# Optimization experiments

Measured on AMD Instinct MI355X. Metric: run time of the kernel, lower is better.

The kernel has to match this reference:

```python
import jax, jax.numpy as jnp
import numpy as np

D_MODEL = 256
D_INNER = 512
D_STATE = 16
DT_RANK = 16
D_CONV = 4
N_LAYERS = 2
L2_LAMBDA = 0.01


def _layernorm(x, g, b, eps=1e-5):
    mu = x.mean(-1, keepdims=True)
    var = x.var(-1, keepdims=True)
    return (x - mu) / jnp.sqrt(var + eps) * g + b


def _selective_scan(u, delta, A, Bm, C, D):
    # u, delta: (B, L, di); A: (di, ds); Bm, C: (B, L, ds); D: (di,)
    B_, L, di = u.shape
    ds = A.shape[1]

    def step(s, inp):
        d_t, u_t, b_t, c_t = inp  # (B,di),(B,di),(B,ds),(B,ds)
        dA = jnp.exp(d_t[..., None] * A)                      # (B,di,ds)
        s = s * dA + (d_t * u_t)[..., None] * b_t[:, None, :]  # (B,di,ds)
        y = jnp.einsum('bds,bs->bd', s, c_t)
        return s, y

    s0 = jnp.zeros((B_, di, ds), u.dtype)
    xs = (jnp.swapaxes(delta, 0, 1), jnp.swapaxes(u, 0, 1),
          jnp.swapaxes(Bm, 0, 1), jnp.swapaxes(C, 0, 1))
    _, ys = jax.lax.scan(step, s0, xs)  # ys: (L, B, di)
    return jnp.swapaxes(ys, 0, 1) + u * D


def _mamba_block(x, ng, nb, ipw, cw, cb, xpw, dtw, dtb, A_log, Dp, opw):
    h = _layernorm(x, ng, nb)
    xz = h @ ipw.T                       # (B,L,2*di)
    u, z = xz[..., :D_INNER], xz[..., D_INNER:]
    # causal depthwise conv along time
    uc = jnp.swapaxes(u, 1, 2)           # (B,di,L)
    uc = jax.lax.conv_general_dilated(
        uc, cw, window_strides=(1,), padding=[(D_CONV - 1, 0)],
        feature_group_count=D_INNER,
        dimension_numbers=('NCH', 'OIH', 'NCH')) + cb[None, :, None]
    u = jax.nn.silu(jnp.swapaxes(uc, 1, 2))
    xdbc = u @ xpw.T                     # (B,L,dt_rank+2*ds)
    dt = xdbc[..., :DT_RANK]
    Bm = xdbc[..., DT_RANK:DT_RANK + D_STATE]
    C = xdbc[..., DT_RANK + D_STATE:]
    delta = jax.nn.softplus(dt @ dtw.T + dtb)
    A = -jnp.exp(A_log)
    y = _selective_scan(u, delta, A, Bm, C, Dp)
    y = y * jax.nn.silu(z)
    return x + y @ opw.T


def setup_inputs() -> dict:
    key = jax.random.key(0)
    ks = jax.random.split(key, 24)
    s = 0.05
    inp = {
        'x': jax.random.normal(ks[0], (4, 1024, 768), jnp.float32),
        'in_w': jax.random.normal(ks[1], (D_MODEL, 768), jnp.float32) * s,
        'in_b': jnp.zeros((D_MODEL,), jnp.float32),
        'ln_g': jnp.ones((D_MODEL,), jnp.float32),
        'ln_b': jnp.zeros((D_MODEL,), jnp.float32),
        'blk_ng': jnp.ones((N_LAYERS, D_MODEL), jnp.float32),
        'blk_nb': jnp.zeros((N_LAYERS, D_MODEL), jnp.float32),
        'blk_ipw': jax.random.normal(ks[2], (N_LAYERS, 2 * D_INNER, D_MODEL), jnp.float32) * s,
        'blk_cw': jax.random.normal(ks[3], (N_LAYERS, D_INNER, 1, D_CONV), jnp.float32) * 0.2,
        'blk_cb': jnp.zeros((N_LAYERS, D_INNER), jnp.float32),
        'blk_xpw': jax.random.normal(ks[4], (N_LAYERS, DT_RANK + 2 * D_STATE, D_INNER), jnp.float32) * s,
        'blk_dtw': jax.random.normal(ks[5], (N_LAYERS, D_INNER, DT_RANK), jnp.float32) * s,
        'blk_dtb': jax.random.normal(ks[6], (N_LAYERS, D_INNER), jnp.float32) * 0.1,
        'blk_Alog': jax.random.uniform(ks[7], (N_LAYERS, D_INNER, D_STATE), jnp.float32, 0.0, 1.0),
        'blk_D': jnp.ones((N_LAYERS, D_INNER), jnp.float32),
        'blk_opw': jax.random.normal(ks[8], (N_LAYERS, D_MODEL, D_INNER), jnp.float32) * s,
        'op_w': jax.random.normal(ks[9], (D_MODEL, D_MODEL), jnp.float32) * s,
        'op_b': jnp.zeros((D_MODEL,), jnp.float32),
        'cls_w': jax.random.normal(ks[10], (128, D_MODEL), jnp.float32) * s,
        'cls_b': jnp.zeros((128,), jnp.float32),
    }
    return inp


def reference(x, in_w, in_b, ln_g, ln_b, blk_ng, blk_nb, blk_ipw, blk_cw, blk_cb,
              blk_xpw, blk_dtw, blk_dtb, blk_Alog, blk_D, blk_opw,
              op_w, op_b, cls_w, cls_b):
    h = x @ in_w.T + in_b
    h = _layernorm(h, ln_g, ln_b)
    h = jax.nn.gelu(h, approximate=False)
    # dropout is identity at inference
    for l in range(N_LAYERS):
        h = _mamba_block(h, blk_ng[l], blk_nb[l], blk_ipw[l], blk_cw[l], blk_cb[l],
                         blk_xpw[l], blk_dtw[l], blk_dtb[l], blk_Alog[l], blk_D[l], blk_opw[l])
    h = h @ op_w.T + op_b
    h = jax.nn.gelu(h, approximate=False)
    logits = h @ cls_w.T + cls_b
    l2_loss = L2_LAMBDA * jnp.mean(jnp.linalg.norm(h, axis=-1))
    return logits, l2_loss
```

## Files before the change

kernel.cpp:

```cpp
#include <hip/hip_runtime.h>
#include <hip/hip_bf16.h>
#include <math.h>

typedef __attribute__((ext_vector_type(8))) short frag8;
typedef __attribute__((ext_vector_type(4))) float f32x4;

__device__ __forceinline__ float gelu_exact(float x) {
    return 0.5f * x * (1.0f + erff(x * 0.70710678118654752f));
}
__device__ __forceinline__ float exp2_raw(float x) {
    return __builtin_amdgcn_exp2f(x);
}
__device__ __forceinline__ float softplus_f(float x) {
    float e = exp2_raw(x * 1.4426950408889634f);
    float sp = __log2f(1.0f + e) * 0.6931471805599453f;
    return (x > 20.0f) ? x : sp;
}
__device__ __forceinline__ float sigmoid_f(float x) {
    return 1.0f / (1.0f + __expf(-x));
}
__device__ __forceinline__ unsigned short bf16bits(float x) {
    __hip_bfloat16 h = __float2bfloat16(x);
    return *(unsigned short*)&h;
}
__device__ __forceinline__ float bf2f(unsigned short u) {
    unsigned int v = ((unsigned int)u) << 16;
    return __builtin_bit_cast(float, v);
}
__device__ __forceinline__ float row_sum16(float x) {
    int t;
    t = __builtin_amdgcn_update_dpp(0, __builtin_bit_cast(int, x), 0x128, 0xf, 0xf, true);
    x += __builtin_bit_cast(float, t);
    t = __builtin_amdgcn_update_dpp(0, __builtin_bit_cast(int, x), 0x124, 0xf, 0xf, true);
    x += __builtin_bit_cast(float, t);
    t = __builtin_amdgcn_update_dpp(0, __builtin_bit_cast(int, x), 0x122, 0xf, 0xf, true);
    x += __builtin_bit_cast(float, t);
    t = __builtin_amdgcn_update_dpp(0, __builtin_bit_cast(int, x), 0x121, 0xf, 0xf, true);
    x += __builtin_bit_cast(float, t);
    return x;
}
__device__ __forceinline__ float prefix_sum64(float x) {
    int t;
    t = __builtin_amdgcn_update_dpp(0, __builtin_bit_cast(int, x), 0x111, 0xf, 0xf, true);
    x += __builtin_bit_cast(float, t);
    t = __builtin_amdgcn_update_dpp(0, __builtin_bit_cast(int, x), 0x112, 0xf, 0xf, true);
    x += __builtin_bit_cast(float, t);
    t = __builtin_amdgcn_update_dpp(0, __builtin_bit_cast(int, x), 0x114, 0xf, 0xf, true);
    x += __builtin_bit_cast(float, t);
    t = __builtin_amdgcn_update_dpp(0, __builtin_bit_cast(int, x), 0x118, 0xf, 0xf, true);
    x += __builtin_bit_cast(float, t);
    t = __builtin_amdgcn_update_dpp(0, __builtin_bit_cast(int, x), 0x142, 0xa, 0xf, true);
    x += __builtin_bit_cast(float, t);
    t = __builtin_amdgcn_update_dpp(0, __builtin_bit_cast(int, x), 0x143, 0xc, 0xf, true);
    x += __builtin_bit_cast(float, t);
    return x;
}

struct CvtArgs {
    const float* src[6];
    unsigned short* dst[6];
    int n4[6];
};
__global__ __launch_bounds__(256)
void cvt_all(CvtArgs a, int total4, const float* __restrict__ Alog,
             float* __restrict__ Ac, float* __restrict__ Z, int zquads, float* l2)
{
    int i = blockIdx.x * 256 + threadIdx.x;
    if (i >= total4) {
        int j = i - total4;
        if (j < 16384) {
            Ac[j] = -__expf(Alog[j]) * 1.4426950408889634f;
        } else {
            int z = j - 16384;
            if (z < zquads) {
                float4 zero = {0.f, 0.f, 0.f, 0.f};
                reinterpret_cast<float4*>(Z)[z] = zero;
            }
        }
        if (j == 0) *l2 = 0.0f;
        return;
    }
    int seg = 0;
    while (i >= a.n4[seg]) { i -= a.n4[seg]; seg++; }
    float4 v = reinterpret_cast<const float4*>(a.src[seg])[i];
    ushort4 o;
    o.x = bf16bits(v.x); o.y = bf16bits(v.y); o.z = bf16bits(v.z); o.w = bf16bits(v.w);
    reinterpret_cast<ushort4*>(a.dst[seg])[i] = o;
}

__global__ __launch_bounds__(256)
void gemm_ipw(const unsigned short* __restrict__ A,
              const unsigned short* __restrict__ W,
              float* __restrict__ xzuT,
              unsigned short* __restrict__ szT)
{
    __shared__ __align__(16) unsigned short As[64][72];
    __shared__ __align__(16) unsigned short Bs[64][72];

    const int tid = threadIdx.x;
    const int wid = tid >> 6, lane = tid & 63;
    const int wm = (wid >> 1) * 32, wn = (wid & 1) * 32;
    const int m0 = blockIdx.y * 64, n0 = blockIdx.x * 64;
    const int lrow = lane & 15, quad = lane >> 4;
    const int K = 256;

    const int sm = tid >> 2;
    const int sk = (tid & 3) * 8;

    f32x4 acc[2][2] = {};

    for (int k0 = 0; k0 < K; k0 += 64) {
        float4 av0 = *reinterpret_cast<const float4*>(A + (size_t)(m0 + sm) * K + k0 + sk);
        float4 av1 = *reinterpret_cast<const float4*>(A + (size_t)(m0 + sm) * K + k0 + sk + 32);
        *reinterpret_cast<float4*>(&As[sm][sk]) = av0;
        *reinterpret_cast<float4*>(&As[sm][sk + 32]) = av1;
        float4 bv0 = *reinterpret_cast<const float4*>(W + (size_t)(n0 + sm) * K + k0 + sk);
        float4 bv1 = *reinterpret_cast<const float4*>(W + (size_t)(n0 + sm) * K + k0 + sk + 32);
        *reinterpret_cast<float4*>(&Bs[sm][sk]) = bv0;
        *reinterpret_cast<float4*>(&Bs[sm][sk + 32]) = bv1;
        __syncthreads();

        #pragma unroll
        for (int h = 0; h < 2; h++) {
            frag8 a0 = *reinterpret_cast<const frag8*>(&As[wm + lrow][h * 32 + quad * 8]);
            frag8 a1 = *reinterpret_cast<const frag8*>(&As[wm + 16 + lrow][h * 32 + quad * 8]);
            frag8 b0 = *reinterpret_cast<const frag8*>(&Bs[wn + lrow][h * 32 + quad * 8]);
            frag8 b1 = *reinterpret_cast<const frag8*>(&Bs[wn + 16 + lrow][h * 32 + quad * 8]);

            acc[0][0] = __builtin_amdgcn_mfma_f32_16x16x32_bf16(a0, b0, acc[0][0], 0, 0, 0);
            acc[0][1] = __builtin_amdgcn_mfma_f32_16x16x32_bf16(a0, b1, acc[0][1], 0, 0, 0);
            acc[1][0] = __builtin_amdgcn_mfma_f32_16x16x32_bf16(a1, b0, acc[1][0], 0, 0, 0);
            acc[1][1] = __builtin_amdgcn_mfma_f32_16x16x32_bf16(a1, b1, acc[1][1], 0, 0, 0);
        }
        __syncthreads();
    }

    const int bb = m0 >> 10;
    const int tb = m0 & 1023;
    #pragma unroll
    for (int mi = 0; mi < 2; mi++) {
        int t4 = tb + wm + mi * 16 + quad * 4;
        #pragma unroll
        for (int nj = 0; nj < 2; nj++) {
            int col = n0 + wn + nj * 16 + lrow;
            if (col < 512) {
                float4 o = { acc[mi][nj][0], acc[mi][nj][1], acc[mi][nj][2], acc[mi][nj][3] };
                *reinterpret_cast<float4*>(xzuT + ((size_t)(bb * 512 + col)) * 1024 + t4) = o;
            } else {
                int z = col - 512;
                ushort4 o;
                float v0 = acc[mi][nj][0], v1 = acc[mi][nj][1], v2 = acc[mi][nj][2], v3 = acc[mi][nj][3];
                o.x = bf16bits(v0 * sigmoid_f(v0));
                o.y = bf16bits(v1 * sigmoid_f(v1));
                o.z = bf16bits(v2 * sigmoid_f(v2));
                o.w = bf16bits(v3 * sigmoid_f(v3));
                *reinterpret_cast<ushort4*>(szT + ((size_t)(bb * 512 + z)) * 1024 + t4) = o;
            }
        }
    }
}

__global__ __launch_bounds__(256)
void gemm_cat(const float* __restrict__ xzuT,
              const unsigned short* __restrict__ W,
              const float* __restrict__ cw, const float* __restrict__ cb,
              float* __restrict__ ucT,
              float* __restrict__ xdt, float* __restrict__ BT, float* __restrict__ CT)
{
    __shared__ __align__(16) unsigned short As[64][72];
    __shared__ __align__(16) unsigned short Bs[64][72];

    const int tid = threadIdx.x;
    const int wid = tid >> 6, lane = tid & 63;
    const int wm = (wid >> 1) * 32, wn = (wid & 1) * 32;
    const int kc = blockIdx.x;
    const int m0 = blockIdx.y * 64;
    const int bb = m0 >> 10;
    const int tb = m0 & 1023;
    const int lrow = lane & 15, quad = lane >> 4;
    const int N = 48;

    const int sm = tid >> 2;
    const int sk = (tid & 3) * 8;

    f32x4 acc[2][2] = {};

    for (int k0 = 0; k0 < 128; k0 += 64) {
        #pragma unroll
        for (int p = 0; p < 4; p++) {
            int kk = (tid >> 4) + p * 16;
            int k  = kc * 128 + k0 + kk;
            int mq = tid & 15;
            int tg = tb + mq * 4;
            const float* rowp = xzuT + ((size_t)(bb * 512 + k)) * 1024;
            float4 cur = *reinterpret_cast<const float4*>(rowp + tg);
            float4 prev = {0.f, 0.f, 0.f, 0.f};
            if (tg != 0) prev = *reinterpret_cast<const float4*>(rowp + tg - 4);
            float4 cv = *reinterpret_cast<const float4*>(cw + k * 4);
            float cbv = cb[k];
            float o0 = cbv + cv.x*prev.y + cv.y*prev.z + cv.z*prev.w + cv.w*cur.x;
            float o1 = cbv + cv.x*prev.z + cv.y*prev.w + cv.z*cur.x  + cv.w*cur.y;
            float o2 = cbv + cv.x*prev.w + cv.y*cur.x  + cv.z*cur.y  + cv.w*cur.z;
            float o3 = cbv + cv.x*cur.x  + cv.y*cur.y  + cv.z*cur.z  + cv.w*cur.w;
            o0 *= sigmoid_f(o0); o1 *= sigmoid_f(o1);
            o2 *= sigmoid_f(o2); o3 *= sigmoid_f(o3);
            float4 uo = { o0, o1, o2, o3 };
            *reinterpret_cast<float4*>(ucT + ((size_t)(bb * 512 + k)) * 1024 + tg) = uo;
            As[mq * 4 + 0][kk] = bf16bits(o0);
            As[mq * 4 + 1][kk] = bf16bits(o1);
            As[mq * 4 + 2][kk] = bf16bits(o2);
            As[mq * 4 + 3][kk] = bf16bits(o3);
        }
        float4 bv0 = {0.f, 0.f, 0.f, 0.f};
        float4 bv1 = {0.f, 0.f, 0.f, 0.f};
        if (sm < N) {
            bv0 = *reinterpret_cast<const float4*>(W + (size_t)sm * 512 + kc * 128 + k0 + sk);
            bv1 = *reinterpret_cast<const float4*>(W + (size_t)sm * 512 + kc * 128 + k0 + sk + 32);
        }
        *reinterpret_cast<float4*>(&Bs[sm][sk]) = bv0;
        *reinterpret_cast<float4*>(&Bs[sm][sk + 32]) = bv1;
        __syncthreads();

        #pragma unroll
        for (int h = 0; h < 2; h++) {
            frag8 a0 = *reinterpret_cast<const frag8*>(&As[wm + lrow][h * 32 + quad * 8]);
            frag8 a1 = *reinterpret_cast<const frag8*>(&As[wm + 16 + lrow][h * 32 + quad * 8]);
            frag8 b0 = *reinterpret_cast<const frag8*>(&Bs[wn + lrow][h * 32 + quad * 8]);
            frag8 b1 = *reinterpret_cast<const frag8*>(&Bs[wn + 16 + lrow][h * 32 + quad * 8]);

            acc[0][0] = __builtin_amdgcn_mfma_f32_16x16x32_bf16(a0, b0, acc[0][0], 0, 0, 0);
            acc[0][1] = __builtin_amdgcn_mfma_f32_16x16x32_bf16(a0, b1, acc[0][1], 0, 0, 0);
            acc[1][0] = __builtin_amdgcn_mfma_f32_16x16x32_bf16(a1, b0, acc[1][0], 0, 0, 0);
            acc[1][1] = __builtin_amdgcn_mfma_f32_16x16x32_bf16(a1, b1, acc[1][1], 0, 0, 0);
        }
        __syncthreads();
    }

    #pragma unroll
    for (int mi = 0; mi < 2; mi++) {
        #pragma unroll
        for (int nj = 0; nj < 2; nj++) {
            int col = wn + nj * 16 + lrow;
            if (col >= N) continue;
            #pragma unroll
            for (int r = 0; r < 4; r++) {
                int trow = tb + wm + mi * 16 + quad * 4 + r;
                float v = acc[mi][nj][r];
                if (col < 16)
                    atomicAdd(&xdt[((size_t)(bb * 1024 + trow)) * 16 + col], v);
                else if (col < 32)
                    atomicAdd(&BT[((size_t)(bb * 16 + col - 16)) * 1024 + trow], v);
                else
                    atomicAdd(&CT[((size_t)(bb * 16 + col - 32)) * 1024 + trow], v);
            }
        }
    }
}

__global__ __launch_bounds__(512)
void rowgemm(const unsigned short* __restrict__ A,
             const float* __restrict__ Af,
             const unsigned short* __restrict__ W,
             const float* __restrict__ bias,
             const float* res,
             const float* g1, const float* b1, int gelu1,
             const float* g2, const float* b2,
             float* outF, unsigned short* outB, float* l2out,
             const unsigned short* clsW, const float* clsB, float* clsOut,
             int K)
{
    __shared__ __align__(16) unsigned short As[16][72];
    __shared__ __align__(16) unsigned short Bs[256][72];
    __shared__ float red[8][16][2];
    __shared__ float sq[16];
    __shared__ __align__(16) unsigned short hb[16][264];

    const int tid = threadIdx.x;
    const int w = tid >> 6, lane = tid & 63;
    const int lrow = lane & 15, quad = lane >> 4;
    const int m0 = blockIdx.x * 16;

    f32x4 acc[2] = {};

    for (int k0 = 0; k0 < K; k0 += 64) {
        if (tid < 64) {
            int r_ = tid >> 2, c8 = (tid & 3) * 8;
            if (Af) {
                const float* src = Af + (size_t)(m0 + r_) * K + k0;
                float4 v0 = *reinterpret_cast<const float4*>(src + c8);
                float4 v1 = *reinterpret_cast<const float4*>(src + c8 + 4);
                float4 v2 = *reinterpret_cast<const float4*>(src + c8 + 32);
                float4 v3 = *reinterpret_cast<const float4*>(src + c8 + 36);
                unsigned short* dst = &As[r_][c8];
                dst[0] = bf16bits(v0.x); dst[1] = bf16bits(v0.y);
                dst[2] = bf16bits(v0.z); dst[3] = bf16bits(v0.w);
                dst[4] = bf16bits(v1.x); dst[5] = bf16bits(v1.y);
                dst[6] = bf16bits(v1.z); dst[7] = bf16bits(v1.w);
                unsigned short* dst2 = &As[r_][c8 + 32];
                dst2[0] = bf16bits(v2.x); dst2[1] = bf16bits(v2.y);
                dst2[2] = bf16bits(v2.z); dst2[3] = bf16bits(v2.w);
                dst2[4] = bf16bits(v3.x); dst2[5] = bf16bits(v3.y);
                dst2[6] = bf16bits(v3.z); dst2[7] = bf16bits(v3.w);
            } else {
                float4 av0 = *reinterpret_cast<const float4*>(A + (size_t)(m0 + r_) * K + k0 + c8);
                float4 av1 = *reinterpret_cast<const float4*>(A + (size_t)(m0 + r_) * K + k0 + c8 + 32);
                *reinterpret_cast<float4*>(&As[r_][c8]) = av0;
                *reinterpret_cast<float4*>(&As[r_][c8 + 32]) = av1;
            }
        }
        #pragma unroll
        for (int i = 0; i < 2; i++) {
            int n = (tid >> 2) + i * 128;
            int c8 = (tid & 3) * 8;
            float4 bv0 = *reinterpret_cast<const float4*>(W + (size_t)n * K + k0 + c8);
            float4 bv1 = *reinterpret_cast<const float4*>(W + (size_t)n * K + k0 + c8 + 32);
            *reinterpret_cast<float4*>(&Bs[n][c8]) = bv0;
            *reinterpret_cast<float4*>(&Bs[n][c8 + 32]) = bv1;
        }
        __syncthreads();
        #pragma unroll
        for (int h = 0; h < 2; h++) {
            frag8 a = *reinterpret_cast<const frag8*>(&As[lrow][h * 32 + quad * 8]);
            #pragma unroll
            for (int nj = 0; nj < 2; nj++) {
                frag8 b = *reinterpret_cast<const frag8*>(&Bs[w * 32 + nj * 16 + lrow][h * 32 + quad * 8]);
                acc[nj] = __builtin_amdgcn_mfma_f32_16x16x32_bf16(a, b, acc[nj], 0, 0, 0);
            }
        }
        __syncthreads();
    }

    float v[2][4];
    #pragma unroll
    for (int nj = 0; nj < 2; nj++) {
        int col = w * 32 + nj * 16 + lrow;
        #pragma unroll
        for (int r = 0; r < 4; r++) {
            int row = m0 + quad * 4 + r;
            float t = acc[nj][r];
            if (bias) t += bias[col];
            if (res) t += res[(size_t)row * 256 + col];
            v[nj][r] = t;
        }
    }

    if (g1) {
        #pragma unroll
        for (int r = 0; r < 4; r++) {
            float s1 = v[0][r] + v[1][r];
            float s2 = v[0][r]*v[0][r] + v[1][r]*v[1][r];
            s1 = row_sum16(s1); s2 = row_sum16(s2);
            if (lrow == 0) { red[w][quad * 4 + r][0] = s1; red[w][quad * 4 + r][1] = s2; }
        }
        __syncthreads();
        #pragma unroll
        for (int r = 0; r < 4; r++) {
            int rr = quad * 4 + r;
            float t1 = 0.f, t2 = 0.f;
            #pragma unroll
            for (int ww = 0; ww < 8; ww++) { t1 += red[ww][rr][0]; t2 += red[ww][rr][1]; }
            float mu = t1 * (1.0f / 256.0f);
            float var = t2 * (1.0f / 256.0f) - mu * mu;
            float rstd = rsqrtf(var + 1e-5f);
            #pragma unroll
            for (int nj = 0; nj < 2; nj++) {
                int col = w * 32 + nj * 16 + lrow;
                float t = (v[nj][r] - mu) * rstd * g1[col] + b1[col];
                if (gelu1) t = gelu_exact(t);
                v[nj][r] = t;
            }
        }
        __syncthreads();
    } else if (gelu1) {
        #pragma unroll
        for (int nj = 0; nj < 2; nj++)
            #pragma unroll
            for (int r = 0; r < 4; r++)
                v[nj][r] = gelu_exact(v[nj][r]);
    }

    if (outF) {
        #pragma unroll
        for (int nj = 0; nj < 2; nj++) {
            int col = w * 32 + nj * 16 + lrow;
            #pragma unroll
            for (int r = 0; r < 4; r++)
                outF[(size_t)(m0 + quad * 4 + r) * 256 + col] = v[nj][r];
        }
    }

    if (l2out) {
        #pragma unroll
        for (int r = 0; r < 4; r++) {
            float s2 = v[0][r]*v[0][r] + v[1][r]*v[1][r];
            s2 = row_sum16(s2);
            if (lrow == 0) red[w][quad * 4 + r][0] = s2;
        }
        __syncthreads();
        if (tid < 16) {
            float t = 0.f;
            #pragma unroll
            for (int ww = 0; ww < 8; ww++) t += red[ww][tid][0];
            sq[tid] = sqrtf(t);
        }
        __syncthreads();
        if (tid == 0) {
            float a = 0.f;
            #pragma unroll
            for (int i = 0; i < 16; i++) a += sq[i];
            atomicAdd(l2out, a * (0.01f / 4096.0f));
        }
    }

    if (g2) {
        __syncthreads();
        #pragma unroll
        for (int r = 0; r < 4; r++) {
            float s1 = v[0][r] + v[1][r];
            float s2 = v[0][r]*v[0][r] + v[1][r]*v[1][r];
            s1 = row_sum16(s1); s2 = row_sum16(s2);
            if (lrow == 0) { red[w][quad * 4 + r][0] = s1; red[w][quad * 4 + r][1] = s2; }
        }
        __syncthreads();
        #pragma unroll
        for (int r = 0; r < 4; r++) {
            int rr = quad * 4 + r;
            float t1 = 0.f, t2 = 0.f;
            #pragma unroll
            for (int ww = 0; ww < 8; ww++) { t1 += red[ww][rr][0]; t2 += red[ww][rr][1]; }
            float mu = t1 * (1.0f / 256.0f);
            float var = t2 * (1.0f / 256.0f) - mu * mu;
            float rstd = rsqrtf(var + 1e-5f);
            #pragma unroll
            for (int nj = 0; nj < 2; nj++) {
                int col = w * 32 + nj * 16 + lrow;
                outB[(size_t)(m0 + rr) * 256 + col] = bf16bits((v[nj][r] - mu) * rstd * g2[col] + b2[col]);
            }
        }
    } else if (outB) {
        #pragma unroll
        for (int nj = 0; nj < 2; nj++) {
            int col = w * 32 + nj * 16 + lrow;
            #pragma unroll
            for (int r = 0; r < 4; r++)
                outB[(size_t)(m0 + quad * 4 + r) * 256 + col] = bf16bits(v[nj][r]);
        }
    }

    if (clsW) {
        #pragma unroll
        for (int nj = 0; nj < 2; nj++) {
            int col = w * 32 + nj * 16 + lrow;
            #pragma unroll
            for (int r = 0; r < 4; r++)
                hb[quad * 4 + r][col] = bf16bits(v[nj][r]);
        }
        __syncthreads();
        f32x4 cacc = {};
        #pragma unroll
        for (int k0 = 0; k0 < 256; k0 += 32) {
            frag8 a = *reinterpret_cast<const frag8*>(&hb[lrow][k0 + quad * 8]);
            frag8 b = *reinterpret_cast<const frag8*>(clsW + (size_t)(w * 16 + lrow) * 256 + k0 + quad * 8);
            cacc = __builtin_amdgcn_mfma_f32_16x16x32_bf16(a, b, cacc, 0, 0, 0);
        }
        int col = w * 16 + lrow;
        float cb = clsB[col];
        #pragma unroll
        for (int r = 0; r < 4; r++)
            clsOut[(size_t)(m0 + quad * 4 + r) * 128 + col] = cacc[r] + cb;
    }
}

__global__ __launch_bounds__(1024)
void scan_chunked(const float* __restrict__ xdt,
                  const float* __restrict__ dtw, const float* __restrict__ dtb,
                  const float* __restrict__ ucT,
                  const float* __restrict__ BT, const float* __restrict__ CT,
                  const unsigned short* __restrict__ szT,
                  const float* __restrict__ Ac,
                  const float* __restrict__ Dp,
                  unsigned short* __restrict__ y)
{
    __shared__ float aprod_s[16][64];
    __shared__ float sfin_s[16][64];
    __shared__ float sin_w[16][64];
    __shared__ __align__(16) float ylocal[16][64][4];
    __shared__ __align__(16) float dltS[4][1032];
    __shared__ __align__(16) float ucS[4][1032];

    const int j = blockIdx.x;
    const int bid = (j & 7) * 64 + (j >> 3);
    const int b = bid >> 7;
    const int d0 = (bid & 127) * 4;
    const int w = threadIdx.x >> 6;
    const int lane = threadIdx.x & 63;
    const int dsub = lane >> 4, s = lane & 15;
    const int d = d0 + dsub;
    const int t = w * 64 + lane;

    const float Acoef = Ac[d * 16 + s];

    const float4* Bp = reinterpret_cast<const float4*>(BT + ((size_t)(b * 16 + s)) * 1024 + w * 64);
    const float4* Cp = reinterpret_cast<const float4*>(CT + ((size_t)(b * 16 + s)) * 1024 + w * 64);

    {
        int dd = lane >> 4, tq = (lane & 15) * 4;
        float4 v = *reinterpret_cast<const float4*>(ucT + ((size_t)(b * 512 + d0 + dd)) * 1024 + w * 64 + tq);
        *reinterpret_cast<float4*>(&ucS[dd][w * 64 + tq]) = v;
    }
    const float* xr = xdt + ((size_t)(b * 1024) + t) * 16;
    float4 x0 = *reinterpret_cast<const float4*>(xr + 0);
    float4 x1 = *reinterpret_cast<const float4*>(xr + 4);
    float4 x2 = *reinterpret_cast<const float4*>(xr + 8);
    float4 x3 = *reinterpret_cast<const float4*>(xr + 12);
    float4 B4 = Bp[0], C4 = Cp[0];
    unsigned short szr[4];
    #pragma unroll
    for (int dd = 0; dd < 4; dd++)
        szr[dd] = szT[((size_t)(b * 512 + d0 + dd)) * 1024 + t];

    #pragma unroll
    for (int dd = 0; dd < 4; dd++) {
        const float* wt = dtw + (size_t)(d0 + dd) * 16;
        float a2 = dtb[d0 + dd]
            + x0.x * wt[0]  + x0.y * wt[1]  + x0.z * wt[2]  + x0.w * wt[3]
            + x1.x * wt[4]  + x1.y * wt[5]  + x1.z * wt[6]  + x1.w * wt[7]
            + x2.x * wt[8]  + x2.y * wt[9]  + x2.z * wt[10] + x2.w * wt[11]
            + x3.x * wt[12] + x3.y * wt[13] + x3.z * wt[14] + x3.w * wt[15];
        dltS[dd][t] = softplus_f(a2);
    }

    float st = 0.0f, ap = 1.0f;
    #pragma unroll
    for (int q = 0; q < 16; q++) {
        float4 nB, nC;
        if (q < 15) { nB = Bp[q + 1]; nC = Cp[q + 1]; }
        float4 dt4 = *reinterpret_cast<const float4*>(&dltS[dsub][w * 64 + q * 4]);
        float4 ut4 = *reinterpret_cast<const float4*>(&ucS[dsub][w * 64 + q * 4]);
        const float* dtp = (const float*)&dt4;
        const float* utp = (const float*)&ut4;
        const float* Btp = (const float*)&B4;
        const float* Ctp = (const float*)&C4;
        #pragma unroll
        for (int jj = 0; jj < 4; jj++) {
            float dA = exp2_raw(dtp[jj] * Acoef);
            st = st * dA + dtp[jj] * utp[jj] * Btp[jj];
            ap *= dA;
            float part = row_sum16(st * Ctp[jj]);
            if (s == 0) ylocal[w][q * 4 + jj][dsub] = part;
        }
        B4 = nB; C4 = nC;
    }
    aprod_s[w][lane] = ap;
    sfin_s[w][lane] = st;
    __syncthreads();

    {
        float pre = 0.0f;
        #pragma unroll
        for (int c = 0; c < 15; c++) {
            float apc = aprod_s[c][lane];
            float sfc = sfin_s[c][lane];
            float cand = sfc + apc * pre;
            pre = (c < w) ? cand : pre;
        }
        sin_w[w][lane] = pre;
    }

    float cums[4];
    #pragma unroll
    for (int dd = 0; dd < 4; dd++)
        cums[dd] = dltS[dd][t];
    #pragma unroll
    for (int dd = 0; dd < 4; dd++)
        cums[dd] = prefix_sum64(cums[dd]);

    float4 yl = *reinterpret_cast<const float4*>(&ylocal[w][lane][0]);
    float acc[4] = { yl.x, yl.y, yl.z, yl.w };

    float Cs[4];
    #pragma unroll
    for (int jj = 0; jj < 4; jj++)
        Cs[jj] = CT[((size_t)(b * 16 + jj)) * 1024 + t];
    #pragma unroll
    for (int sq = 0; sq < 4; sq++) {
        float Csn[4];
        if (sq < 3) {
            #pragma unroll
            for (int jj = 0; jj < 4; jj++)
                Csn[jj] = CT[((size_t)(b * 16 + (sq + 1) * 4 + jj)) * 1024 + t];
        }
        #pragma unroll
        for (int dd = 0; dd < 4; dd++) {
            float4 sin4 = *reinterpret_cast<const float4*>(&sin_w[w][dd * 16 + sq * 4]);
            const float* sp = (const float*)&sin4;
            #pragma unroll
            for (int jj = 0; jj < 4; jj++) {
                float ac = Ac[(d0 + dd) * 16 + sq * 4 + jj];
                acc[dd] += sp[jj] * Cs[jj] * exp2_raw(ac * cums[dd]);
            }
        }
        #pragma unroll
        for (int jj = 0; jj < 4; jj++) Cs[jj] = Csn[jj];
    }

    const size_t row = (size_t)b * 1024 + t;
    ushort4 yo;
    {
        float ut0 = ucS[0][t], ut1 = ucS[1][t], ut2 = ucS[2][t], ut3 = ucS[3][t];
        float y0 = (acc[0] + ut0 * Dp[d0 + 0]) * bf2f(szr[0]);
        float y1 = (acc[1] + ut1 * Dp[d0 + 1]) * bf2f(szr[1]);
        float y2 = (acc[2] + ut2 * Dp[d0 + 2]) * bf2f(szr[2]);
        float y3 = (acc[3] + ut3 * Dp[d0 + 3]) * bf2f(szr[3]);
        yo.x = bf16bits(y0); yo.y = bf16bits(y1);
        yo.z = bf16bits(y2); yo.w = bf16bits(y3);
    }
    *reinterpret_cast<ushort4*>(y + row * 512 + d0) = yo;
}

extern "C" void kernel_launch(void* const* d_in, const int* in_sizes, int n_in,
                              void* d_out, int out_size, void* d_ws, size_t ws_size,
                              hipStream_t stream)
{
    const float* x      = (const float*)d_in[0];
    const float* in_b   = (const float*)d_in[2];
    const float* ln_g   = (const float*)d_in[3];
    const float* ln_b   = (const float*)d_in[4];
    const float* blk_ng  = (const float*)d_in[5];
    const float* blk_nb  = (const float*)d_in[6];
    const float* blk_cw  = (const float*)d_in[8];
    const float* blk_cb  = (const float*)d_in[9];
    const float* blk_dtw = (const float*)d_in[11];
    const float* blk_dtb = (const float*)d_in[12];
    const float* blk_Alog= (const float*)d_in[13];
    const float* blk_D   = (const float*)d_in[14];
    const float* op_b   = (const float*)d_in[17];
    const float* cls_b  = (const float*)d_in[19];
    float* out = (float*)d_out;

    const int BL = 4096;
    float* ws = (float*)d_ws;
    float* h0   = ws;
    float* xzuT = h0 + 1048576;
    float* ucT  = xzuT + 2097152;
    float* xdt  = ucT + 2097152;
    float* BT   = xdt + 131072;
    float* CT   = BT + 131072;
    float* Ac   = CT + 131072;
    unsigned short* szT = (unsigned short*)(Ac + 16384);
    unsigned short* wb  = szT + 2097152;
    unsigned short* hnb = wb + 1130496;
    unsigned short* ybb = hnb + 1048576;
    unsigned short* h0b = hnb;
    unsigned short* in_wb  = wb;
    unsigned short* ipw_b  = wb + 196608;
    unsigned short* xpw_b  = wb + 720896;
    unsigned short* opw_b  = wb + 770048;
    unsigned short* op_wb  = wb + 1032192;
    unsigned short* cls_wb = wb + 1097728;

    CvtArgs ca;
    ca.src[0] = (const float*)d_in[1];  ca.dst[0] = in_wb;  ca.n4[0] = 196608 / 4;
    ca.src[1] = (const float*)d_in[7];  ca.dst[1] = ipw_b;  ca.n4[1] = 524288 / 4;
    ca.src[2] = (const float*)d_in[10]; ca.dst[2] = xpw_b;  ca.n4[2] = 49152 / 4;
    ca.src[3] = (const float*)d_in[15]; ca.dst[3] = opw_b;  ca.n4[3] = 262144 / 4;
    ca.src[4] = (const float*)d_in[16]; ca.dst[4] = op_wb;  ca.n4[4] = 65536 / 4;
    ca.src[5] = (const float*)d_in[18]; ca.dst[5] = cls_wb; ca.n4[5] = 32768 / 4;
    int total4 = 1130496 / 4;
    int zquads = 393216 / 4;
    int totalg = total4 + 16384 + zquads;
    cvt_all<<<(totalg + 255) / 256, 256, 0, stream>>>(ca, total4, blk_Alog, Ac,
                                                      xdt, zquads,
                                                      out + (size_t)BL * 128);

    rowgemm<<<256, 512, 0, stream>>>(nullptr, x, in_wb, in_b, nullptr,
                                     ln_g, ln_b, 1,
                                     blk_ng, blk_nb,
                                     h0, hnb, nullptr,
                                     nullptr, nullptr, nullptr, 768);

    for (int l = 0; l < 2; l++) {
        const float* cw   = blk_cw  + (size_t)l * 512 * 4;
        const float* cb   = blk_cb  + l * 512;
        const float* dtw  = blk_dtw + (size_t)l * 512 * 16;
        const float* dtb  = blk_dtb + l * 512;
        const float* Dl   = blk_D   + l * 512;
        const unsigned short* ipwl = ipw_b + (size_t)l * 262144;
        const unsigned short* xpwl = xpw_b + (size_t)l * 24576;
        const unsigned short* opwl = opw_b + (size_t)l * 131072;
        float* xdtl = xdt + (size_t)l * 65536;
        float* BTl  = BT  + (size_t)l * 65536;
        float* CTl  = CT  + (size_t)l * 65536;

        gemm_ipw<<<dim3(16, 64), 256, 0, stream>>>(hnb, ipwl, xzuT, szT);
        gemm_cat<<<dim3(4, 64), 256, 0, stream>>>(xzuT, xpwl, cw, cb, ucT, xdtl, BTl, CTl);
        scan_chunked<<<512, 1024, 0, stream>>>(xdtl, dtw, dtb, ucT, BTl, CTl, szT,
                                               Ac + (size_t)l * 8192, Dl, ybb);
        if (l == 0)
            rowgemm<<<256, 512, 0, stream>>>(ybb, nullptr, opwl, nullptr, h0,
                                             nullptr, nullptr, 0,
                                             blk_ng + 256, blk_nb + 256,
                                             h0, hnb, nullptr,
                                             nullptr, nullptr, nullptr, 512);
        else
            rowgemm<<<256, 512, 0, stream>>>(ybb, nullptr, opwl, nullptr, h0,
                                             nullptr, nullptr, 0,
                                             nullptr, nullptr,
                                             nullptr, h0b, nullptr,
                                             nullptr, nullptr, nullptr, 512);
    }

    rowgemm<<<256, 512, 0, stream>>>(h0b, nullptr, op_wb, op_b, nullptr,
                                     nullptr, nullptr, 1,
                                     nullptr, nullptr,
                                     nullptr, nullptr, out + (size_t)BL * 128,
                                     cls_wb, cls_b, out, 256);
}
```

Before: 283.2 us.

## Rewrite selective scan as time-parallel wave scans with carried chunk state

```diff
diff --git a/kernel.cpp b/kernel.cpp
--- a/kernel.cpp
+++ b/kernel.cpp
@@ -39,22 +39,37 @@
     x += __builtin_bit_cast(float, t);
     return x;
 }
-__device__ __forceinline__ float prefix_sum64(float x) {
-    int t;
-    t = __builtin_amdgcn_update_dpp(0, __builtin_bit_cast(int, x), 0x111, 0xf, 0xf, true);
-    x += __builtin_bit_cast(float, t);
-    t = __builtin_amdgcn_update_dpp(0, __builtin_bit_cast(int, x), 0x112, 0xf, 0xf, true);
-    x += __builtin_bit_cast(float, t);
-    t = __builtin_amdgcn_update_dpp(0, __builtin_bit_cast(int, x), 0x114, 0xf, 0xf, true);
-    x += __builtin_bit_cast(float, t);
-    t = __builtin_amdgcn_update_dpp(0, __builtin_bit_cast(int, x), 0x118, 0xf, 0xf, true);
-    x += __builtin_bit_cast(float, t);
-    t = __builtin_amdgcn_update_dpp(0, __builtin_bit_cast(int, x), 0x142, 0xa, 0xf, true);
-    x += __builtin_bit_cast(float, t);
-    t = __builtin_amdgcn_update_dpp(0, __builtin_bit_cast(int, x), 0x143, 0xc, 0xf, true);
-    x += __builtin_bit_cast(float, t);
-    return x;
-}
+
+#define SCAN_STEP(A, Bq, ctrl, rmask)                                          \
+    {                                                                          \
+        int ta_ = __builtin_amdgcn_update_dpp(0x3f800000,                      \
+                      __builtin_bit_cast(int, A), ctrl, rmask, 0xf, false);    \
+        int tb_ = __builtin_amdgcn_update_dpp(0,                               \
+                      __builtin_bit_cast(int, Bq), ctrl, rmask, 0xf, false);   \
+        float fa_ = __builtin_bit_cast(float, ta_);                            \
+        float fb_ = __builtin_bit_cast(float, tb_);                            \
+        Bq = fmaf(A, fb_, Bq);                                                 \
+        A  = A * fa_;                                                          \
+    }
+
+#define SCAN64(A, Bq)            \
+    SCAN_STEP(A, Bq, 0x111, 0xf) \
+    SCAN_STEP(A, Bq, 0x112, 0xf) \
+    SCAN_STEP(A, Bq, 0x114, 0xf) \
+    SCAN_STEP(A, Bq, 0x118, 0xf) \
+    SCAN_STEP(A, Bq, 0x142, 0xa) \
+    SCAN_STEP(A, Bq, 0x143, 0xc)
+
+#define SCHAIN(AcS, Bv, Cv, cr)                                                \
+    {                                                                          \
+        float A  = exp2_raw(dt_c * AcS);                                       \
+        float Bq = du * Bv;                                                    \
+        SCAN64(A, Bq)                                                          \
+        float st = fmaf(A, cr, Bq);                                            \
+        cr = __builtin_bit_cast(float,                                         \
+             __builtin_amdgcn_readlane(__builtin_bit_cast(int, st), 63));      \
+        yacc = fmaf(Cv, st, yacc);                                             \
+    }
 
 struct CvtArgs {
     const float* src[6];
@@ -481,12 +496,9 @@
                   const float* __restrict__ Dp,
                   unsigned short* __restrict__ y)
 {
-    __shared__ float aprod_s[16][64];
-    __shared__ float sfin_s[16][64];
-    __shared__ float sin_w[16][64];
-    __shared__ __align__(16) float ylocal[16][64][4];
     __shared__ __align__(16) float dltS[4][1032];
     __shared__ __align__(16) float ucS[4][1032];
+    __shared__ __align__(16) float yl[4][1032];
 
     const int j = blockIdx.x;
     const int bid = (j & 7) * 64 + (j >> 3);
@@ -494,14 +506,10 @@
     const int d0 = (bid & 127) * 4;
     const int w = threadIdx.x >> 6;
     const int lane = threadIdx.x & 63;
-    const int dsub = lane >> 4, s = lane & 15;
-    const int d = d0 + dsub;
-    const int t = w * 64 + lane;
-
-    const float Acoef = Ac[d * 16 + s];
-
-    const float4* Bp = reinterpret_cast<const float4*>(BT + ((size_t)(b * 16 + s)) * 1024 + w * 64);
-    const float4* Cp = reinterpret_cast<const float4*>(CT + ((size_t)(b * 16 + s)) * 1024 + w * 64);
+    const int t = threadIdx.x;
+
+    #pragma unroll
+    for (int dd = 0; dd < 4; dd++) yl[dd][t] = 0.0f;
 
     {
         int dd = lane >> 4, tq = (lane & 15) * 4;
@@ -513,7 +521,6 @@
     float4 x1 = *reinterpret_cast<const float4*>(xr + 4);
     float4 x2 = *reinterpret_cast<const float4*>(xr + 8);
     float4 x3 = *reinterpret_cast<const float4*>(xr + 12);
-    float4 B4 = Bp[0], C4 = Cp[0];
     unsigned short szr[4];
     #pragma unroll
     for (int dd = 0; dd < 4; dd++)
@@ -529,89 +536,60 @@
             + x3.x * wt[12] + x3.y * wt[13] + x3.z * wt[14] + x3.w * wt[15];
         dltS[dd][t] = softplus_f(a2);
     }
-
-    float st = 0.0f, ap = 1.0f;
-    #pragma unroll
-    for (int q = 0; q < 16; q++) {
-        float4 nB, nC;
-        if (q < 15) { nB = Bp[q + 1]; nC = Cp[q + 1]; }
-        float4 dt4 = *reinterpret_cast<const float4*>(&dltS[dsub][w * 64 + q * 4]);
-        float4 ut4 = *reinterpret_cast<const float4*>(&ucS[dsub][w * 64 + q * 4]);
-        const float* dtp = (const float*)&dt4;
-        const float* utp = (const float*)&ut4;
-        const float* Btp = (const float*)&B4;
-        const float* Ctp = (const float*)&C4;
-        #pragma unroll
-        for (int jj = 0; jj < 4; jj++) {
-            float dA = exp2_raw(dtp[jj] * Acoef);
-            st = st * dA + dtp[jj] * utp[jj] * Btp[jj];
-            ap *= dA;
-            float part = row_sum16(st * Ctp[jj]);
-            if (s == 0) ylocal[w][q * 4 + jj][dsub] = part;
-        }
-        B4 = nB; C4 = nC;
-    }
-    aprod_s[w][lane] = ap;
-    sfin_s[w][lane] = st;
     __syncthreads();
 
-    {
-        float pre = 0.0f;
-        #pragma unroll
-        for (int c = 0; c < 15; c++) {
-            float apc = aprod_s[c][lane];
-            float sfc = sfin_s[c][lane];
-            float cand = sfc + apc * pre;
-            pre = (c < w) ? cand : pre;
-        }
-        sin_w[w][lane] = pre;
-    }
-
-    float cums[4];
-    #pragma unroll
-    for (int dd = 0; dd < 4; dd++)
-        cums[dd] = dltS[dd][t];
-    #pragma unroll
-    for (int dd = 0; dd < 4; dd++)
-        cums[dd] = prefix_sum64(cums[dd]);
-
-    float4 yl = *reinterpret_cast<const float4*>(&ylocal[w][lane][0]);
-    float acc[4] = { yl.x, yl.y, yl.z, yl.w };
-
-    float Cs[4];
-    #pragma unroll
-    for (int jj = 0; jj < 4; jj++)
-        Cs[jj] = CT[((size_t)(b * 16 + jj)) * 1024 + t];
-    #pragma unroll
-    for (int sq = 0; sq < 4; sq++) {
-        float Csn[4];
-        if (sq < 3) {
-            #pragma unroll
-            for (int jj = 0; jj < 4; jj++)
-                Csn[jj] = CT[((size_t)(b * 16 + (sq + 1) * 4 + jj)) * 1024 + t];
-        }
-        #pragma unroll
-        for (int dd = 0; dd < 4; dd++) {
-            float4 sin4 = *reinterpret_cast<const float4*>(&sin_w[w][dd * 16 + sq * 4]);
-            const float* sp = (const float*)&sin4;
-            #pragma unroll
-            for (int jj = 0; jj < 4; jj++) {
-                float ac = Ac[(d0 + dd) * 16 + sq * 4 + jj];
-                acc[dd] += sp[jj] * Cs[jj] * exp2_raw(ac * cums[dd]);
-            }
-        }
-        #pragma unroll
-        for (int jj = 0; jj < 4; jj++) Cs[jj] = Csn[jj];
-    }
+    const int dI = w & 3;
+    const int sB = (w >> 2) * 4;
+    const float A0c = Ac[(d0 + dI) * 16 + sB + 0];
+    const float A1c = Ac[(d0 + dI) * 16 + sB + 1];
+    const float A2c = Ac[(d0 + dI) * 16 + sB + 2];
+    const float A3c = Ac[(d0 + dI) * 16 + sB + 3];
+    const float* B0p = BT + ((size_t)(b * 16 + sB + 0)) * 1024;
+    const float* B1p = BT + ((size_t)(b * 16 + sB + 1)) * 1024;
+    const float* B2p = BT + ((size_t)(b * 16 + sB + 2)) * 1024;
+    const float* B3p = BT + ((size_t)(b * 16 + sB + 3)) * 1024;
+    const float* C0p = CT + ((size_t)(b * 16 + sB + 0)) * 1024;
+    const float* C1p = CT + ((size_t)(b * 16 + sB + 1)) * 1024;
+    const float* C2p = CT + ((size_t)(b * 16 + sB + 2)) * 1024;
+    const float* C3p = CT + ((size_t)(b * 16 + sB + 3)) * 1024;
+
+    float cr0 = 0.f, cr1 = 0.f, cr2 = 0.f, cr3 = 0.f;
+    float dt_c = dltS[dI][lane];
+    float uu_c = ucS[dI][lane];
+    float Bv0 = B0p[lane], Bv1 = B1p[lane], Bv2 = B2p[lane], Bv3 = B3p[lane];
+    float Cv0 = C0p[lane], Cv1 = C1p[lane], Cv2 = C2p[lane], Cv3 = C3p[lane];
+
+    for (int c = 0; c < 16; ++c) {
+        float dt_n = 0.f, uu_n = 0.f;
+        float Bn0 = 0.f, Bn1 = 0.f, Bn2 = 0.f, Bn3 = 0.f;
+        float Cn0 = 0.f, Cn1 = 0.f, Cn2 = 0.f, Cn3 = 0.f;
+        if (c < 15) {
+            int tn = (c + 1) * 64 + lane;
+            dt_n = dltS[dI][tn]; uu_n = ucS[dI][tn];
+            Bn0 = B0p[tn]; Bn1 = B1p[tn]; Bn2 = B2p[tn]; Bn3 = B3p[tn];
+            Cn0 = C0p[tn]; Cn1 = C1p[tn]; Cn2 = C2p[tn]; Cn3 = C3p[tn];
+        }
+        float du = dt_c * uu_c;
+        float yacc = 0.0f;
+        SCHAIN(A0c, Bv0, Cv0, cr0)
+        SCHAIN(A1c, Bv1, Cv1, cr1)
+        SCHAIN(A2c, Bv2, Cv2, cr2)
+        SCHAIN(A3c, Bv3, Cv3, cr3)
+        atomicAdd(&yl[dI][c * 64 + lane], yacc);
+        dt_c = dt_n; uu_c = uu_n;
+        Bv0 = Bn0; Bv1 = Bn1; Bv2 = Bn2; Bv3 = Bn3;
+        Cv0 = Cn0; Cv1 = Cn1; Cv2 = Cn2; Cv3 = Cn3;
+    }
+    __syncthreads();
 
     const size_t row = (size_t)b * 1024 + t;
     ushort4 yo;
     {
         float ut0 = ucS[0][t], ut1 = ucS[1][t], ut2 = ucS[2][t], ut3 = ucS[3][t];
-        float y0 = (acc[0] + ut0 * Dp[d0 + 0]) * bf2f(szr[0]);
-        float y1 = (acc[1] + ut1 * Dp[d0 + 1]) * bf2f(szr[1]);
-        float y2 = (acc[2] + ut2 * Dp[d0 + 2]) * bf2f(szr[2]);
-        float y3 = (acc[3] + ut3 * Dp[d0 + 3]) * bf2f(szr[3]);
+        float y0 = (yl[0][t] + ut0 * Dp[d0 + 0]) * bf2f(szr[0]);
+        float y1 = (yl[1][t] + ut1 * Dp[d0 + 1]) * bf2f(szr[1]);
+        float y2 = (yl[2][t] + ut2 * Dp[d0 + 2]) * bf2f(szr[2]);
+        float y3 = (yl[3][t] + ut3 * Dp[d0 + 3]) * bf2f(szr[3]);
         yo.x = bf16bits(y0); yo.y = bf16bits(y1);
         yo.z = bf16bits(y2); yo.w = bf16bits(y3);
     }
```

Result: slower. 314.7 us (+11.1%).
